# Kernel optimization log

Measured on AMD Instinct MI355X. Metric: run time of the kernel, lower is better.

Reference implementation:

```python
import jax, jax.numpy as jnp
import numpy as np

# ---- layer config (yolov3, layer_no=2) ----
STRIDE = 8
N_CLASSES = 80
IGNORE_TH = 0.7
ANCHORS_PX = np.array([[10,13],[16,30],[33,23],[30,61],[62,45],[59,119],[116,90],[156,198],[373,326]], np.float32)
ALL_ANCHORS = ANCHORS_PX / STRIDE          # [9,2] in grid units
ANCHOR_ID_LO, ANCHOR_ID_HI = 0, 2          # anchor_mask[2] = [0,1,2]
ANCHORS = ALL_ANCHORS[ANCHOR_ID_LO:ANCHOR_ID_HI+1]  # [3,2]
NA = 3
NC = N_CLASSES + 5

B, IN_CH, NG, NBOX = 16, 256, 76, 50


def _safe_log(p):
    # emulate torch BCE's log clamp at -100; eps stops 0*inf -> nan
    return jnp.maximum(jnp.log(jnp.maximum(p, 1e-12)), -100.0)


def _bce_sum(p, t, w=None):
    l = -(t * _safe_log(p) + (1.0 - t) * _safe_log(1.0 - p))
    if w is not None:
        l = l * w
    return l.sum()


def setup_inputs() -> dict:
    key = jax.random.key(0)
    k1, k2, k3, k4, k5 = jax.random.split(key, 5)
    xin = jax.random.normal(k1, (B, IN_CH, NG, NG), jnp.float32)
    cls = jax.random.randint(k2, (B, NBOX, 1), 0, N_CLASSES).astype(jnp.float32)
    cxy = jax.random.uniform(k3, (B, NBOX, 2), jnp.float32, 0.02, 0.98)
    wh = jax.random.uniform(k4, (B, NBOX, 2), jnp.float32, 0.02, 0.40)
    labels = jnp.concatenate([cls, cxy, wh], axis=-1)  # [B,N,5]
    W = jax.random.normal(k5, (NA * NC, IN_CH), jnp.float32) * 0.02  # 1x1 conv
    b = jnp.zeros((NA * NC,), jnp.float32)
    return {"xin": xin, "labels": labels, "W": W, "b": b}


def _yolo_loss(xin, labels, W, b):
    nB, _, nG, _ = xin.shape
    anchors = jnp.asarray(ANCHORS, xin.dtype)          # [3,2]
    all_anchors = jnp.asarray(ALL_ANCHORS, xin.dtype)  # [9,2]

    # 1x1 conv -> [B, A, G, G, C]
    x = jnp.einsum('bchw,oc->bohw', xin, W) + b[None, :, None, None]
    x = x.reshape(nB, NA, NC, nG, nG).transpose(0, 1, 3, 4, 2)

    xy = jax.nn.sigmoid(x[..., :2])
    wh = x[..., 2:4]
    conf_cls = jax.nn.sigmoid(x[..., 4:])  # [B,A,G,G,1+ncls]

    gy, gx = jnp.meshgrid(jnp.arange(nG, dtype=x.dtype), jnp.arange(nG, dtype=x.dtype), indexing='ij')
    pred_boxes = jnp.stack([
        xy[..., 0] + gx,
        xy[..., 1] + gy,
        jnp.exp(wh[..., 0]) * anchors[:, 0][None, :, None, None],
        jnp.exp(wh[..., 1]) * anchors[:, 1][None, :, None, None]], axis=-1)  # [B,A,G,G,4]

    # ---- ground truth ----
    valid = labels.sum(-1) > 0                     # [B,N]
    gt_cls = labels[..., 0].astype(jnp.int32)
    gt = labels[..., 1:] * nG                      # [B,N,4] cx,cy,w,h in grid units
    gt_x, gt_y, gt_w, gt_h = gt[..., 0], gt[..., 1], gt[..., 2], gt[..., 3]
    gi = jnp.floor(gt_x).astype(jnp.int32)
    gj = jnp.floor(gt_y).astype(jnp.int32)

    # best anchor per gt: wh-IoU vs all 9 anchors (centered at origin)
    inter_a = jnp.minimum(gt_w[..., None], all_anchors[:, 0]) * jnp.minimum(gt_h[..., None], all_anchors[:, 1])
    union_a = gt_w[..., None] * gt_h[..., None] + all_anchors[:, 0] * all_anchors[:, 1] - inter_a
    best = jnp.argmax(inter_a / union_a, axis=-1)  # [B,N]
    in_mask = (best >= ANCHOR_ID_LO) & (best <= ANCHOR_ID_HI)
    a = jnp.where(in_mask, best % 3, -1)           # [B,N]

    # all-pairs IoU: pred boxes vs gt boxes (ignore mask)
    pb = pred_boxes.reshape(nB, -1, 4)             # [B,M,4], M = A*G*G
    pa_area = pb[..., 2] * pb[..., 3]
    gt_area = gt_w * gt_h
    tl = jnp.maximum(pb[:, :, None, :2] - pb[:, :, None, 2:] / 2, gt[:, None, :, :2] - gt[:, None, :, 2:] / 2)
    br = jnp.minimum(pb[:, :, None, :2] + pb[:, :, None, 2:] / 2, gt[:, None, :, :2] + gt[:, None, :, 2:] / 2)
    inter = jnp.prod(br - tl, -1) * jnp.all(tl < br, -1)
    iou = inter / (pa_area[:, :, None] + gt_area[:, None, :] - inter)
    iou = jnp.where(valid[:, None, :], iou, 0.0)
    best_iou = iou.max(-1)                         # [B,M]
    has_boxes = valid.any(-1)
    obj_mask = jnp.where(has_boxes[:, None], best_iou <= IGNORE_TH, True).reshape(nB, NA, nG, nG)

    # ---- scatter target assignment ----
    assign = valid & (a >= 0)
    a_safe = jnp.clip(a, 0, NA - 1)
    aw = anchors[a_safe, 0]
    ah = anchors[a_safe, 1]
    tvec = jnp.concatenate([
        (gt_x - jnp.floor(gt_x))[..., None],
        (gt_y - jnp.floor(gt_y))[..., None],
        jnp.log(gt_w / aw + 1e-16)[..., None],
        jnp.log(gt_h / ah + 1e-16)[..., None],
        jnp.ones_like(gt_x)[..., None],
        jax.nn.one_hot(gt_cls, N_CLASSES, dtype=x.dtype)], axis=-1)  # [B,N,NC]
    sval = 2.0 - gt_w * gt_h / (nG * nG)

    bf = jnp.broadcast_to(jnp.arange(nB)[:, None], a.shape).reshape(-1)
    af = jnp.where(assign, a_safe, NA).reshape(-1)  # NA is OOB -> dropped
    jf = gj.reshape(-1)
    if_ = gi.reshape(-1)

    target = jnp.zeros((nB, NA, nG, nG, NC), x.dtype).at[bf, af, jf, if_].set(tvec.reshape(-1, NC), mode='drop')
    scale = jnp.zeros((nB, NA, nG, nG), x.dtype).at[bf, af, jf, if_].set(sval.reshape(-1), mode='drop')
    obj_mask = obj_mask.at[bf, af, jf, if_].set(True, mode='drop')
    noobj = jnp.zeros((nB, NA, nG, nG), bool).at[bf, af, jf, if_].set(True, mode='drop')

    # ---- losses ----
    nm = noobj.astype(x.dtype)[..., None]
    p_obj = conf_cls[..., 0] * obj_mask
    t_obj = target[..., 4] * obj_mask
    p_xy = xy * nm
    t_xy = target[..., :2] * nm
    p_wh = wh * nm
    t_wh = target[..., 2:4] * nm
    p_cls = conf_cls[..., 1:] * nm
    t_cls = target[..., 5:] * nm
    sc = scale[..., None]

    loss_xy = _bce_sum(p_xy, t_xy, sc)
    rs = jnp.sqrt(sc)
    loss_wh = 0.5 * jnp.sum((p_wh * rs - t_wh * rs) ** 2)
    loss_obj = _bce_sum(p_obj, t_obj)
    loss_cls = _bce_sum(p_cls, t_cls)
    loss = loss_xy + loss_wh + loss_obj + loss_cls
    return jnp.stack([loss, loss_xy, loss_wh, loss_obj, loss_cls])


def reference(xin, labels, W, b):
    return _yolo_loss(xin, labels, W, b)
```

## Files before the change

kernel.cpp:

```cpp
#include <hip/hip_runtime.h>
#include <math.h>

#define NB    16
#define NAg   3
#define NCg   85
#define NCLS  80
#define NGg   76
#define NSp   (NGg*NGg)
#define NBOX  50
#define INCH  256

#define ACC_OFF  0
#define HAS_OFF  32
#define WT_OFF   128
#define GB_OFF   (WT_OFF + 16384)
#define GA_OFF   (GB_OFF + 25600)
#define GI_OFF   (GA_OFF + 25600)

__device__ __constant__ float c_AW[9] = {1.25f,2.0f,4.125f,3.75f,7.75f,7.375f,14.5f,19.5f,46.625f};
__device__ __constant__ float c_AH[9] = {1.625f,3.75f,2.875f,7.625f,5.625f,14.875f,11.25f,24.75f,40.75f};

__device__ __forceinline__ float safe_log(float p) {
    return fmaxf(logf(fmaxf(p, 1e-12f)), -100.0f);
}
__device__ __forceinline__ float sigm(float x) {
    return 1.0f / (1.0f + expf(-x));
}

__global__ __launch_bounds__(256) void k_labels(
    const float* __restrict__ labels, const float* __restrict__ W,
    float* __restrict__ Wt, float* __restrict__ gbox, float* __restrict__ gaux,
    int* __restrict__ gint, int* __restrict__ hasAny, float* __restrict__ acc)
{
    const int b = blockIdx.x, tid = threadIdx.x;
    const int t = b * 256 + tid;

    {
        const int c = t >> 4, f = t & 15;
        Wt[t] = (f < 15) ? W[((f / 5) * NCg + (f % 5)) * INCH + c] : 0.f;
    }
    if (b == 0 && tid < 8) acc[tid] = 0.f;

    int valid = 0;
    if (tid < NBOX) {
        const int bt = b * NBOX + tid;
        const float* L = labels + (size_t)bt * 5;
        const float l0 = L[0], l1 = L[1], l2 = L[2], l3 = L[3], l4 = L[4];
        valid = (l0 + l1 + l2 + l3 + l4) > 0.f;

        const float gx = l1 * NGg, gy = l2 * NGg, gw = l3 * NGg, gh = l4 * NGg;

        int best = 0; float brr = -1.f;
#pragma unroll
        for (int k = 0; k < 9; k++) {
            float inter = fminf(gw, c_AW[k]) * fminf(gh, c_AH[k]);
            float uni   = gw*gh + c_AW[k]*c_AH[k] - inter;
            float r     = inter / uni;
            if (r > brr) { brr = r; best = k; }
        }
        const int a = (best <= 2) ? best : -1;
        const int assign = valid && (a >= 0);
        const int a_safe = a < 0 ? 0 : (a > 2 ? 2 : a);

        const int gi = (int)floorf(gx), gj = (int)floorf(gy);
        const int inb = (gi >= 0) && (gi < NGg) && (gj >= 0) && (gj < NGg);
        const int cell = (assign && inb) ? (a * NSp + gj * NGg + gi) : -1;

        float* gb = gbox + (size_t)bt * 8;
        gb[0] = gx - gw * 0.5f;
        gb[1] = gy - gh * 0.5f;
        gb[2] = gx + gw * 0.5f;
        gb[3] = gy + gh * 0.5f;
        gb[4] = valid ? gw * gh : -1.f;
        gb[5] = __int_as_float(cell);

        float* ga = gaux + (size_t)bt * 8;
        ga[0] = gx - floorf(gx);
        ga[1] = gy - floorf(gy);
        ga[2] = logf(gw / c_AW[a_safe] + 1e-16f);
        ga[3] = logf(gh / c_AH[a_safe] + 1e-16f);
        ga[4] = 2.f - gw * gh / (float)NSp;

        gint[bt*2 + 0] = cell;
        gint[bt*2 + 1] = (int)l0;
    }
    if (tid < 64) {
        const unsigned long long m = __ballot(valid != 0);
        if (tid == 0) hasAny[b] = (m != 0ULL) ? 1 : 0;
    }
}

__global__ __launch_bounds__(256) void k_main(
    const float* __restrict__ xin, const float* __restrict__ Wt,
    const float* __restrict__ bias, const float* __restrict__ gbox,
    const int* __restrict__ hasAny, float* __restrict__ acc)
{
    __shared__ float partial[15 * 256];
    __shared__ float red[15 * 64];
    __shared__ int   smask[256];

    const int b   = blockIdx.y;
    const int tid = threadIdx.x;
    const int w   = tid >> 6, l = tid & 63;
    const int s   = blockIdx.x * 64 + l;
    const bool live = (s < NSp);

    float accv[15];
#pragma unroll
    for (int f = 0; f < 15; ++f) accv[f] = 0.f;

    if (live) {
        const float* xp = xin + ((size_t)b * INCH + w * 64) * NSp + s;
        const float* wp = Wt + (w * 64) * 16;
#pragma unroll 2
        for (int c0 = 0; c0 < 64; c0 += 8) {
            float v[8];
#pragma unroll
            for (int k = 0; k < 8; ++k) v[k] = xp[(size_t)(c0 + k) * NSp];
#pragma unroll
            for (int k = 0; k < 8; ++k) {
                const float* wr = wp + ((c0 + k) << 4);
#pragma unroll
                for (int f = 0; f < 15; ++f) accv[f] += wr[f] * v[k];
            }
        }
    }
#pragma unroll
    for (int f = 0; f < 15; ++f) partial[f * 256 + tid] = accv[f];
    __syncthreads();

    for (int f = w; f < 15; f += 4) {
        red[f * 64 + l] = partial[f * 256 + l]       + partial[f * 256 + 64 + l]
                        + partial[f * 256 + 128 + l] + partial[f * 256 + 192 + l];
    }
    __syncthreads();

    float cf[3];
    int mask = 0;
    if (live) {
        const int sy = s / NGg;
        const int sx = s - sy * NGg;
        const float gxf = (float)sx, gyf = (float)sy;

        float pbx0[3], pby0[3], pbx1[3], pby1[3], pa[3];
#pragma unroll
        for (int a = 0; a < 3; ++a) {
            const float x0 = red[(a*5+0) * 64 + l];
            const float x1 = red[(a*5+1) * 64 + l];
            const float x2 = red[(a*5+2) * 64 + l];
            const float x3 = red[(a*5+3) * 64 + l];
            const float x4 = red[(a*5+4) * 64 + l];
            const float px = sigm(x0 + bias[a*NCg+0]) + gxf;
            const float py = sigm(x1 + bias[a*NCg+1]) + gyf;
            const float pw = expf(x2 + bias[a*NCg+2]) * c_AW[a];
            const float ph = expf(x3 + bias[a*NCg+3]) * c_AH[a];
            cf[a]   = sigm(x4 + bias[a*NCg+4]);
            pbx0[a] = px - pw * 0.5f;  pby0[a] = py - ph * 0.5f;
            pbx1[a] = px + pw * 0.5f;  pby1[a] = py + ph * 0.5f;
            pa[a]   = pw * ph;
        }

        const float* gb = gbox + (size_t)b * NBOX * 8;
        for (int n = w; n < NBOX; n += 4) {
            const float bx0 = gb[n*8+0], by0 = gb[n*8+1];
            const float bx1 = gb[n*8+2], by1 = gb[n*8+3];
            const float gar = gb[n*8+4];
            const int cell  = __float_as_int(gb[n*8+5]);
            const int d = cell - s;
            if (d == 0)       mask |= 8;
            if (d == NSp)     mask |= 16;
            if (d == 2*NSp)   mask |= 32;
            if (gar >= 0.f) {
#pragma unroll
                for (int a = 0; a < 3; ++a) {
                    const float tlx = fmaxf(pbx0[a], bx0);
                    const float tly = fmaxf(pby0[a], by0);
                    const float brx = fminf(pbx1[a], bx1);
                    const float bry = fminf(pby1[a], by1);
                    const float dx = brx - tlx, dy = bry - tly;
                    const float inter = (dx > 0.f && dy > 0.f) ? dx * dy : 0.f;
                    if (inter > 0.7f * (pa[a] + gar - inter)) mask |= (1 << a);
                }
            }
        }
    }
    smask[tid] = mask;
    __syncthreads();

    if (w == 0) {
        float lsum = 0.f;
        if (live) {
            const int m = smask[l] | smask[64 + l] | smask[128 + l] | smask[192 + l];
            const bool hasB = hasAny[b] != 0;
#pragma unroll
            for (int a = 0; a < 3; ++a) {
                const bool ex = (m & (1 << a)) != 0;
                const bool as = (m & (8 << a)) != 0;
                const bool maskpre = hasB ? (!ex) : true;
                if (maskpre || as) {
                    const float c = cf[a];
                    lsum += as ? -safe_log(c) : -safe_log(1.f - c);
                }
            }
        }
#pragma unroll
        for (int off = 32; off > 0; off >>= 1) lsum += __shfl_down(lsum, off);
        if (l == 0) atomicAdd(&acc[2], lsum);
    }
}

__global__ __launch_bounds__(256) void k_assigned(
    const float* __restrict__ xin, const float* __restrict__ W,
    const float* __restrict__ bias, const float* __restrict__ gaux,
    const int* __restrict__ gint, float* __restrict__ acc)
{
    const int t = blockIdx.x;
    const int b = t / NBOX, n = t % NBOX;
    const int tid = threadIdx.x;

    __shared__ int   scell[NBOX];
    __shared__ float4 col4[64];
    __shared__ float  xsh[NCg];
    __shared__ float  sacc[3];

    if (tid < NBOX) scell[tid] = gint[(b * NBOX + tid) * 2];
    __syncthreads();

    const int cell = scell[n];
    if (cell < 0) return;
    for (int n2 = n + 1; n2 < NBOX; ++n2)
        if (scell[n2] == cell) return;

    const int a = cell / NSp, s = cell % NSp;
    const int o0 = a * NCg;

    ((float*)col4)[tid] = xin[((size_t)b * INCH + tid) * NSp + s];
    if (tid < 3) sacc[tid] = 0.f;
    __syncthreads();

    const int wid = tid >> 6, lane = tid & 63;
    for (int o = wid; o < NCg; o += 4) {
        const float4 wv = *(const float4*)&W[(size_t)(o0 + o) * INCH + lane * 4];
        const float4 cv = col4[lane];
        float p = wv.x*cv.x + wv.y*cv.y + wv.z*cv.z + wv.w*cv.w;
        for (int off = 32; off; off >>= 1) p += __shfl_down(p, off);
        if (lane == 0) xsh[o] = p + bias[o0 + o];
    }
    __syncthreads();

    if (tid < NCg) {
        const float* ga = gaux + (size_t)t * 8;
        const float sval = ga[4];
        const int gcls = gint[t*2 + 1];
        float val = xsh[tid];
        float term; int slot;
        if (tid < 2) {
            float tgt = ga[tid];
            float p = sigm(val);
            term = -(tgt * safe_log(p) + (1.f - tgt) * safe_log(1.f - p)) * sval;
            slot = 0;
        } else if (tid < 4) {
            float tgt = ga[tid];
            float d = val - tgt;
            term = 0.5f * sval * d * d;
            slot = 1;
        } else if (tid == 4) {
            term = 0.f; slot = 2;
        } else {
            float tgt = ((tid - 5) == gcls) ? 1.f : 0.f;
            float p = sigm(val);
            term = -(tgt * safe_log(p) + (1.f - tgt) * safe_log(1.f - p));
            slot = 2;
        }
        atomicAdd(&sacc[slot], term);
    }
    __syncthreads();
    if (tid == 0) {
        atomicAdd(&acc[0], sacc[0]);
        atomicAdd(&acc[1], sacc[1]);
        atomicAdd(&acc[3], sacc[2]);
    }
}

__global__ void k_final(const float* __restrict__ acc, float* __restrict__ out)
{
    float xy = acc[0], wh = acc[1], ob = acc[2], cl = acc[3];
    out[0] = xy + wh + ob + cl;
    out[1] = xy; out[2] = wh; out[3] = ob; out[4] = cl;
}

extern "C" void kernel_launch(void* const* d_in, const int* in_sizes, int n_in,
                              void* d_out, int out_size, void* d_ws, size_t ws_size,
                              hipStream_t stream)
{
    const float* xin    = (const float*)d_in[0];
    const float* labels = (const float*)d_in[1];
    const float* W      = (const float*)d_in[2];
    const float* bias   = (const float*)d_in[3];

    char* ws = (char*)d_ws;
    float* acc    = (float*)(ws + ACC_OFF);
    int*   hasAny = (int*)  (ws + HAS_OFF);
    float* Wt     = (float*)(ws + WT_OFF);
    float* gbox   = (float*)(ws + GB_OFF);
    float* gaux   = (float*)(ws + GA_OFF);
    int*   gint   = (int*)  (ws + GI_OFF);
    float* out    = (float*)d_out;

    k_labels<<<16, 256, 0, stream>>>(labels, W, Wt, gbox, gaux, gint, hasAny, acc);

    k_main<<<dim3((NSp + 63) / 64, NB), 256, 0, stream>>>(xin, Wt, bias, gbox, hasAny, acc);

    k_assigned<<<dim3(NB * NBOX), 256, 0, stream>>>(xin, W, bias, gaux, gint, acc);

    k_final<<<1, 1, 0, stream>>>(acc, out);
}
```

Baseline: 231.7 us.

## Process two spatial positions per thread with float2 loads in main conv kernel

Each thread in k_main now computes the 15 needed conv channels for two adjacent spatial positions using float2 loads, so a block covers 128 positions and weight loads are reused across both. The cross-wave reduction is rebuilt around a float2 shared buffer. The IoU mask loop now runs all 50 boxes in one thread per position instead of splitting boxes across waves, which removes the mask-merge sync. The block count halves, which lowers occupancy and adds more serial per-thread work in the box loop.

Result: faster. 194.3 us (-16.1%).

```diff
diff --git a/kernel.cpp b/kernel.cpp
--- a/kernel.cpp
+++ b/kernel.cpp
@@ -9,6 +9,9 @@
 #define NSp   (NGg*NGg)
 #define NBOX  50
 #define INCH  256
+#define NG2   (NSp/2)
+#define SPB   128
+#define GPB   64
 
 #define ACC_OFF  0
 #define HAS_OFF  32
@@ -95,78 +98,82 @@
     const float* __restrict__ bias, const float* __restrict__ gbox,
     const int* __restrict__ hasAny, float* __restrict__ acc)
 {
-    __shared__ float partial[15 * 256];
-    __shared__ float red[15 * 64];
-    __shared__ int   smask[256];
+    __shared__ float2 buf[4][15][GPB];
+    __shared__ float  wred[2];
 
     const int b   = blockIdx.y;
     const int tid = threadIdx.x;
     const int w   = tid >> 6, l = tid & 63;
-    const int s   = blockIdx.x * 64 + l;
-    const bool live = (s < NSp);
-
-    float accv[15];
-#pragma unroll
-    for (int f = 0; f < 15; ++f) accv[f] = 0.f;
-
-    if (live) {
-        const float* xp = xin + ((size_t)b * INCH + w * 64) * NSp + s;
-        const float* wp = Wt + (w * 64) * 16;
+    const int wu  = __builtin_amdgcn_readfirstlane(w);
+    const int G   = blockIdx.x * GPB + l;
+    const bool liveG = (G < NG2);
+
+    float2 a2[15];
+#pragma unroll
+    for (int f = 0; f < 15; ++f) a2[f] = make_float2(0.f, 0.f);
+
+    if (liveG) {
+        const float* xp = xin + ((size_t)b * INCH + (wu << 6)) * NSp + (G << 1);
+        const float* wp = Wt + ((wu << 6) << 4);
 #pragma unroll 2
         for (int c0 = 0; c0 < 64; c0 += 8) {
-            float v[8];
-#pragma unroll
-            for (int k = 0; k < 8; ++k) v[k] = xp[(size_t)(c0 + k) * NSp];
+            float2 v[8];
+#pragma unroll
+            for (int k = 0; k < 8; ++k)
+                v[k] = *(const float2*)(xp + (size_t)(c0 + k) * NSp);
 #pragma unroll
             for (int k = 0; k < 8; ++k) {
                 const float* wr = wp + ((c0 + k) << 4);
 #pragma unroll
-                for (int f = 0; f < 15; ++f) accv[f] += wr[f] * v[k];
+                for (int f = 0; f < 15; ++f) {
+                    a2[f].x += wr[f] * v[k].x;
+                    a2[f].y += wr[f] * v[k].y;
+                }
             }
         }
     }
 #pragma unroll
-    for (int f = 0; f < 15; ++f) partial[f * 256 + tid] = accv[f];
-    __syncthreads();
-
-    for (int f = w; f < 15; f += 4) {
-        red[f * 64 + l] = partial[f * 256 + l]       + partial[f * 256 + 64 + l]
-                        + partial[f * 256 + 128 + l] + partial[f * 256 + 192 + l];
-    }
-    __syncthreads();
-
-    float cf[3];
-    int mask = 0;
-    if (live) {
-        const int sy = s / NGg;
-        const int sx = s - sy * NGg;
+    for (int f = 0; f < 15; ++f) buf[w][f][l] = a2[f];
+    __syncthreads();
+
+    float lsum = 0.f;
+    const int p = blockIdx.x * SPB + tid;
+    if (tid < SPB && p < NSp) {
+        const int g = tid >> 1, e = tid & 1;
+        float xv[15];
+#pragma unroll
+        for (int f = 0; f < 15; ++f) {
+            xv[f] = ((const float*)&buf[0][f][g])[e]
+                  + ((const float*)&buf[1][f][g])[e]
+                  + ((const float*)&buf[2][f][g])[e]
+                  + ((const float*)&buf[3][f][g])[e];
+        }
+
+        const int sy = p / NGg;
+        const int sx = p - sy * NGg;
         const float gxf = (float)sx, gyf = (float)sy;
 
-        float pbx0[3], pby0[3], pbx1[3], pby1[3], pa[3];
+        float pbx0[3], pby0[3], pbx1[3], pby1[3], pa[3], cf[3];
 #pragma unroll
         for (int a = 0; a < 3; ++a) {
-            const float x0 = red[(a*5+0) * 64 + l];
-            const float x1 = red[(a*5+1) * 64 + l];
-            const float x2 = red[(a*5+2) * 64 + l];
-            const float x3 = red[(a*5+3) * 64 + l];
-            const float x4 = red[(a*5+4) * 64 + l];
-            const float px = sigm(x0 + bias[a*NCg+0]) + gxf;
-            const float py = sigm(x1 + bias[a*NCg+1]) + gyf;
-            const float pw = expf(x2 + bias[a*NCg+2]) * c_AW[a];
-            const float ph = expf(x3 + bias[a*NCg+3]) * c_AH[a];
-            cf[a]   = sigm(x4 + bias[a*NCg+4]);
+            const float px = sigm(xv[a*5+0] + bias[a*NCg+0]) + gxf;
+            const float py = sigm(xv[a*5+1] + bias[a*NCg+1]) + gyf;
+            const float pw = expf(xv[a*5+2] + bias[a*NCg+2]) * c_AW[a];
+            const float ph = expf(xv[a*5+3] + bias[a*NCg+3]) * c_AH[a];
+            cf[a]   = sigm(xv[a*5+4] + bias[a*NCg+4]);
             pbx0[a] = px - pw * 0.5f;  pby0[a] = py - ph * 0.5f;
             pbx1[a] = px + pw * 0.5f;  pby1[a] = py + ph * 0.5f;
             pa[a]   = pw * ph;
         }
 
+        int mask = 0;
         const float* gb = gbox + (size_t)b * NBOX * 8;
-        for (int n = w; n < NBOX; n += 4) {
+        for (int n = 0; n < NBOX; ++n) {
             const float bx0 = gb[n*8+0], by0 = gb[n*8+1];
             const float bx1 = gb[n*8+2], by1 = gb[n*8+3];
             const float gar = gb[n*8+4];
             const int cell  = __float_as_int(gb[n*8+5]);
-            const int d = cell - s;
+            const int d = cell - p;
             if (d == 0)       mask |= 8;
             if (d == NSp)     mask |= 16;
             if (d == 2*NSp)   mask |= 32;
@@ -183,30 +190,25 @@
                 }
             }
         }
-    }
-    smask[tid] = mask;
-    __syncthreads();
-
-    if (w == 0) {
-        float lsum = 0.f;
-        if (live) {
-            const int m = smask[l] | smask[64 + l] | smask[128 + l] | smask[192 + l];
-            const bool hasB = hasAny[b] != 0;
-#pragma unroll
-            for (int a = 0; a < 3; ++a) {
-                const bool ex = (m & (1 << a)) != 0;
-                const bool as = (m & (8 << a)) != 0;
-                const bool maskpre = hasB ? (!ex) : true;
-                if (maskpre || as) {
-                    const float c = cf[a];
-                    lsum += as ? -safe_log(c) : -safe_log(1.f - c);
-                }
+
+        const bool hasB = hasAny[b] != 0;
+#pragma unroll
+        for (int a = 0; a < 3; ++a) {
+            const bool ex = (mask & (1 << a)) != 0;
+            const bool as = (mask & (8 << a)) != 0;
+            const bool maskpre = hasB ? (!ex) : true;
+            if (maskpre || as) {
+                const float c = cf[a];
+                lsum += as ? -safe_log(c) : -safe_log(1.f - c);
             }
         }
-#pragma unroll
-        for (int off = 32; off > 0; off >>= 1) lsum += __shfl_down(lsum, off);
-        if (l == 0) atomicAdd(&acc[2], lsum);
-    }
+    }
+
+#pragma unroll
+    for (int off = 32; off > 0; off >>= 1) lsum += __shfl_down(lsum, off);
+    if (w < 2 && l == 0) wred[w] = lsum;
+    __syncthreads();
+    if (tid == 0) atomicAdd(&acc[2], wred[0] + wred[1]);
 }
 
 __global__ __launch_bounds__(256) void k_assigned(
@@ -309,7 +311,7 @@
 
     k_labels<<<16, 256, 0, stream>>>(labels, W, Wt, gbox, gaux, gint, hasAny, acc);
 
-    k_main<<<dim3((NSp + 63) / 64, NB), 256, 0, stream>>>(xin, Wt, bias, gbox, hasAny, acc);
+    k_main<<<dim3((NSp + SPB - 1) / SPB, NB), 256, 0, stream>>>(xin, Wt, bias, gbox, hasAny, acc);
 
     k_assigned<<<dim3(NB * NBOX), 256, 0, stream>>>(xin, W, bias, gaux, gint, acc);
 
```
